# Optimization experiments

Hardware: AMD Instinct MI355X
Metric: run time of the kernel (lower is better)

The kernel has to match this reference:

```python
import jax, jax.numpy as jnp
import numpy as np

IN_FEATURES = 4096
OUT_FEATURES = 4096
INQ = IN_FEATURES // 4
OUTQ = OUT_FEATURES // 4


def setup_inputs() -> dict:
    key = jax.random.key(0)
    kx, krr, kri, krj, krk, kb = jax.random.split(key, 6)
    scale = 1.0 / np.sqrt(INQ)
    x = jax.random.normal(kx, (8192, IN_FEATURES), dtype=jnp.float32)
    W_rr = jax.random.uniform(krr, (OUTQ, INQ), jnp.float32, -scale, scale)
    # ri/rj/rk weights are scaled by 0.5 at init in the original module
    W_ri = jax.random.uniform(kri, (OUTQ, INQ), jnp.float32, -scale, scale) * 0.5
    W_rj = jax.random.uniform(krj, (OUTQ, INQ), jnp.float32, -scale, scale) * 0.5
    W_rk = jax.random.uniform(krk, (OUTQ, INQ), jnp.float32, -scale, scale) * 0.5
    b_rr = jax.random.uniform(kb, (OUTQ,), jnp.float32, -scale, scale)
    return {"x": x, "W_rr": W_rr, "W_ri": W_ri, "W_rj": W_rj, "W_rk": W_rk, "b_rr": b_rr}


def reference(x, W_rr, W_ri, W_rj, W_rk, b_rr):
    B, F = x.shape
    q = F // 4
    # Stack the four quaternion components: Xc[c] = component c, shape (4, B, q)
    Xc = x.reshape(B, 4, q).transpose(1, 0, 2)
    # Apply each quarter-sized linear to all four components at once.
    Rr = jnp.einsum('cbi,oi->cbo', Xc, W_rr) + b_rr  # linear_rr (with bias)
    Ri = jnp.einsum('cbi,oi->cbo', Xc, W_ri)         # linear_ri
    Rj = jnp.einsum('cbi,oi->cbo', Xc, W_rj)         # linear_rj
    Rk = jnp.einsum('cbi,oi->cbo', Xc, W_rk)         # linear_rk
    # Hamilton-product style combination
    out_r = Rr[0] - Ri[1] - Rj[2] - Rk[3]
    out_i = Ri[0] + Rr[1] + Rk[2] - Rj[3]
    out_j = Rj[0] - Rk[1] + Rr[2] + Ri[3]
    out_k = Rk[0] + Rj[1] - Ri[2] + Rr[3]
    # torch.stack(dim=1).view(B,-1) == concat along features
    return jnp.concatenate([out_r, out_i, out_j, out_k], axis=1)
```

## Files before the change

kernel.cpp:

```cpp
#include <hip/hip_runtime.h>
#include <hip/hip_bf16.h>
#include <stdint.h>

#define M_DIM 8192
#define K_DIM 4096
#define N_DIM 4096
#define QO 1024
#define BM 256
#define BN 128
#define BK 32
#define FBM 128
#define FBN 128

typedef __bf16 bf16x8_t __attribute__((ext_vector_type(8)));
typedef float f32x4_t __attribute__((ext_vector_type(4)));

__device__ __forceinline__ uint32_t f2bf_rne(float f) {
    union { float f; uint32_t u; } v; v.f = f;
    return (v.u + 0x7FFFu + ((v.u >> 16) & 1u)) >> 16;
}
__device__ __forceinline__ uint32_t pack2bf(float lo, float hi) {
    return f2bf_rne(lo) | (f2bf_rne(hi) << 16);
}

__global__ __launch_bounds__(256) void cvt_x_kernel(const float* __restrict__ x,
                                                    uint16_t* __restrict__ xb, int n8) {
    int i = blockIdx.x * 256 + threadIdx.x;
    if (i >= n8) return;
    float4 v0 = ((const float4*)x)[2 * i];
    float4 v1 = ((const float4*)x)[2 * i + 1];
    uint4 o;
    o.x = pack2bf(v0.x, v0.y);
    o.y = pack2bf(v0.z, v0.w);
    o.z = pack2bf(v1.x, v1.y);
    o.w = pack2bf(v1.z, v1.w);
    ((uint4*)xb)[i] = o;
}

__global__ __launch_bounds__(256) void build_w_kernel(
    const float* __restrict__ wrr, const float* __restrict__ wri,
    const float* __restrict__ wrj, const float* __restrict__ wrk,
    uint16_t* __restrict__ wb, int n8) {
    int g = blockIdx.x * 256 + threadIdx.x;
    if (g >= n8) return;
    int n  = g >> 9;
    int k8 = (g & 511) << 3;
    int cp = n >> 10, o = n & 1023;
    int c  = k8 >> 10, i = k8 & 1023;
    int tsel = cp ^ c;
    const float* w = (tsel == 0) ? wrr : (tsel == 1) ? wri : (tsel == 2) ? wrj : wrk;
    float s = ((0x428Eu >> ((cp << 2) | c)) & 1u) ? -1.0f : 1.0f;
    const float* p = w + (size_t)o * QO + i;
    float4 v0 = ((const float4*)p)[0];
    float4 v1 = ((const float4*)p)[1];
    uint4 ob;
    ob.x = pack2bf(s * v0.x, s * v0.y);
    ob.y = pack2bf(s * v0.z, s * v0.w);
    ob.z = pack2bf(s * v1.x, s * v1.y);
    ob.w = pack2bf(s * v1.z, s * v1.w);
    ((uint4*)wb)[g] = ob;
}

__global__ __launch_bounds__(256, 2) void qgemm256_kernel(
    const uint16_t* __restrict__ Abf, const uint16_t* __restrict__ Bbf,
    const float* __restrict__ bias, float* __restrict__ C)
{
    __shared__ uint16_t lA[BM * BK];
    __shared__ uint16_t lB[BN * BK];
    const int t    = threadIdx.x;
    const int wave = t >> 6;
    const int lane = t & 63;
    const int bn = blockIdx.x, bm = blockIdx.y;
    const int wm = wave >> 1, wn = wave & 1;

    f32x4_t acc[8][4];
#pragma unroll
    for (int a = 0; a < 8; ++a)
#pragma unroll
        for (int b = 0; b < 4; ++b)
            acc[a][b] = (f32x4_t){0.f, 0.f, 0.f, 0.f};

    const int fr  = lane & 15;
    const int fkb = (lane >> 4) << 3;
    const uint16_t* pA[8];
    const uint16_t* pB[4];
#pragma unroll
    for (int i = 0; i < 8; ++i)
        pA[i] = lA + (wm * 128 + i * 16 + fr) * BK + fkb;
#pragma unroll
    for (int i = 0; i < 4; ++i)
        pB[i] = lB + (wn * 64 + i * 16 + fr) * BK + fkb;

    const int srow = lane >> 2;
    const int scol = (lane & 3) << 3;
    const uint16_t* gA0 = Abf + (size_t)(bm * BM + wave * 64 + srow) * K_DIM + scol;
    const uint16_t* gB0 = Bbf + (size_t)(bn * BN + wave * 32 + srow) * K_DIM + scol;
    uint16_t* lA0 = lA + wave * 64 * BK;
    uint16_t* lB0 = lB + wave * 32 * BK;

#pragma unroll 1
    for (int kb = 0; kb < K_DIM; kb += BK) {
#pragma unroll
        for (int i = 0; i < 4; ++i)
            __builtin_amdgcn_global_load_lds(
                (const __attribute__((address_space(1))) void*)(gA0 + (size_t)i * 16 * K_DIM + kb),
                (__attribute__((address_space(3))) void*)(lA0 + i * 16 * BK), 16, 0, 0);
#pragma unroll
        for (int i = 0; i < 2; ++i)
            __builtin_amdgcn_global_load_lds(
                (const __attribute__((address_space(1))) void*)(gB0 + (size_t)i * 16 * K_DIM + kb),
                (__attribute__((address_space(3))) void*)(lB0 + i * 16 * BK), 16, 0, 0);
        __syncthreads();

        bf16x8_t bfr[4];
#pragma unroll
        for (int i = 0; i < 4; ++i)
            bfr[i] = *(const bf16x8_t*)pB[i];
#pragma unroll
        for (int mi = 0; mi < 8; ++mi) {
            bf16x8_t af = *(const bf16x8_t*)pA[mi];
#pragma unroll
            for (int ni = 0; ni < 4; ++ni)
                acc[mi][ni] = __builtin_amdgcn_mfma_f32_16x16x32_bf16(
                    af, bfr[ni], acc[mi][ni], 0, 0, 0);
        }
        __syncthreads();
    }

    const int row0 = bm * BM + wm * 128 + ((lane >> 4) << 2);
    const int col0 = bn * BN + wn * 64 + (lane & 15);
#pragma unroll
    for (int ni = 0; ni < 4; ++ni) {
        const int col = col0 + ni * 16;
        const float bv = bias[col & (QO - 1)];
#pragma unroll
        for (int mi = 0; mi < 8; ++mi) {
            const int r = row0 + mi * 16;
            float* cptr = C + (size_t)r * N_DIM + col;
#pragma unroll
            for (int rr = 0; rr < 4; ++rr)
                cptr[(size_t)rr * N_DIM] = acc[mi][ni][rr] + bv;
        }
    }
}

__global__ __launch_bounds__(256) void qgemm_fb_kernel(
    const float* __restrict__ x,
    const float* __restrict__ wrr, const float* __restrict__ wri,
    const float* __restrict__ wrj, const float* __restrict__ wrk,
    const float* __restrict__ bias, float* __restrict__ C)
{
    __shared__ uint16_t lA[FBM * BK];
    __shared__ uint16_t lB[FBN * BK];
    const int t    = threadIdx.x;
    const int wave = t >> 6;
    const int lane = t & 63;
    const int bn = blockIdx.x, bm = blockIdx.y;
    const int wm = wave >> 1, wn = wave & 1;

    f32x4_t acc[4][4];
#pragma unroll
    for (int a = 0; a < 4; ++a)
#pragma unroll
        for (int b = 0; b < 4; ++b)
            acc[a][b] = (f32x4_t){0.f, 0.f, 0.f, 0.f};

    const int fr  = lane & 15;
    const int fkb = (lane >> 4) << 3;
    const uint16_t* pA[4];
    const uint16_t* pB[4];
#pragma unroll
    for (int i = 0; i < 4; ++i) {
        pA[i] = lA + (wm * 64 + i * 16 + fr) * BK + fkb;
        pB[i] = lB + (wn * 64 + i * 16 + fr) * BK + fkb;
    }

    const int mr = t >> 1;
    const int mc = (t & 1) << 4;
    int ng = bn * FBN + mr;
    int bcp = ng >> 10;
    int bo  = ng & 1023;

#pragma unroll 1
    for (int kb = 0; kb < K_DIM; kb += BK) {
        const float* pa = x + (size_t)(bm * FBM + mr) * K_DIM + kb + mc;
        float4 a0 = ((const float4*)pa)[0], a1 = ((const float4*)pa)[1],
               a2 = ((const float4*)pa)[2], a3 = ((const float4*)pa)[3];
        uint4 wv0 = make_uint4(pack2bf(a0.x, a0.y), pack2bf(a0.z, a0.w),
                               pack2bf(a1.x, a1.y), pack2bf(a1.z, a1.w));
        uint4 wv1 = make_uint4(pack2bf(a2.x, a2.y), pack2bf(a2.z, a2.w),
                               pack2bf(a3.x, a3.y), pack2bf(a3.z, a3.w));
        *(uint4*)(lA + mr * BK + mc)     = wv0;
        *(uint4*)(lA + mr * BK + mc + 8) = wv1;

        int k0 = kb + mc;
        int c  = k0 >> 10, ii = k0 & 1023;
        int tsel = bcp ^ c;
        const float* w = (tsel == 0) ? wrr : (tsel == 1) ? wri : (tsel == 2) ? wrj : wrk;
        float s = ((0x428Eu >> ((bcp << 2) | c)) & 1u) ? -1.0f : 1.0f;
        const float* pb = w + (size_t)bo * QO + ii;
        float4 b0 = ((const float4*)pb)[0], b1 = ((const float4*)pb)[1],
               b2 = ((const float4*)pb)[2], b3 = ((const float4*)pb)[3];
        uint4 u0 = make_uint4(pack2bf(s * b0.x, s * b0.y), pack2bf(s * b0.z, s * b0.w),
                              pack2bf(s * b1.x, s * b1.y), pack2bf(s * b1.z, s * b1.w));
        uint4 u1 = make_uint4(pack2bf(s * b2.x, s * b2.y), pack2bf(s * b2.z, s * b2.w),
                              pack2bf(s * b3.x, s * b3.y), pack2bf(s * b3.z, s * b3.w));
        *(uint4*)(lB + mr * BK + mc)     = u0;
        *(uint4*)(lB + mr * BK + mc + 8) = u1;
        __syncthreads();

        bf16x8_t af[4], bfr[4];
#pragma unroll
        for (int i = 0; i < 4; ++i) {
            af[i]  = *(const bf16x8_t*)pA[i];
            bfr[i] = *(const bf16x8_t*)pB[i];
        }
#pragma unroll
        for (int mi = 0; mi < 4; ++mi)
#pragma unroll
            for (int ni = 0; ni < 4; ++ni)
                acc[mi][ni] = __builtin_amdgcn_mfma_f32_16x16x32_bf16(
                    af[mi], bfr[ni], acc[mi][ni], 0, 0, 0);
        __syncthreads();
    }

    const int row0 = bm * FBM + wm * 64 + ((lane >> 4) << 2);
    const int col0 = bn * FBN + wn * 64 + (lane & 15);
#pragma unroll
    for (int ni = 0; ni < 4; ++ni) {
        const int col = col0 + ni * 16;
        const float bv = bias[col & (QO - 1)];
#pragma unroll
        for (int mi = 0; mi < 4; ++mi) {
            const int r = row0 + mi * 16;
            float* cptr = C + (size_t)r * N_DIM + col;
#pragma unroll
            for (int rr = 0; rr < 4; ++rr)
                cptr[(size_t)rr * N_DIM] = acc[mi][ni][rr] + bv;
        }
    }
}

extern "C" void kernel_launch(void* const* d_in, const int* in_sizes, int n_in,
                              void* d_out, int out_size, void* d_ws, size_t ws_size,
                              hipStream_t stream) {
    const float* x   = (const float*)d_in[0];
    const float* wrr = (const float*)d_in[1];
    const float* wri = (const float*)d_in[2];
    const float* wrj = (const float*)d_in[3];
    const float* wrk = (const float*)d_in[4];
    const float* brr = (const float*)d_in[5];
    float* out = (float*)d_out;

    const size_t xb_bytes = (size_t)M_DIM * K_DIM * 2;
    const size_t wb_bytes = (size_t)N_DIM * K_DIM * 2;

    if (ws_size >= xb_bytes + wb_bytes) {
        uint16_t* xb = (uint16_t*)d_ws;
        uint16_t* wb = (uint16_t*)((char*)d_ws + xb_bytes);
        const int nx8 = M_DIM * K_DIM / 8;
        cvt_x_kernel<<<nx8 / 256, 256, 0, stream>>>(x, xb, nx8);
        const int nw8 = N_DIM * K_DIM / 8;
        build_w_kernel<<<nw8 / 256, 256, 0, stream>>>(wrr, wri, wrj, wrk, wb, nw8);
        dim3 grid(N_DIM / BN, M_DIM / BM);
        qgemm256_kernel<<<grid, 256, 0, stream>>>(xb, wb, brr, out);
    } else {
        dim3 grid(N_DIM / FBN, M_DIM / FBM);
        qgemm_fb_kernel<<<grid, 256, 0, stream>>>(x, wrr, wri, wrj, wrk, brr, out);
    }
}
```

Measured before the change: 544.6 us.

## Rewrite bf16 GEMM as 256x256 double-buffered 8-wave pipelined kernel with swizzled LDS

Replaces the 256x128 single-buffered GEMM with a 512-thread 256x256x64 tile kernel. It double-buffers LDS with direct global-to-LDS loads split into four phases, interleaving fragment reads, next-tile staging and MFMA work, with s_setprio around the MFMAs. LDS addresses are XOR-swizzled to avoid bank conflicts, and a block-index swizzle improves L2 reuse. The two conversion kernels are merged into one launch. The cost is higher register and LDS pressure (128KB shared) and more complex barrier and waitcnt logic.

```diff
diff --git a/kernel.cpp b/kernel.cpp
--- a/kernel.cpp
+++ b/kernel.cpp
@@ -1,16 +1,22 @@
 #include <hip/hip_runtime.h>
-#include <hip/hip_bf16.h>
 #include <stdint.h>
 
 #define M_DIM 8192
 #define K_DIM 4096
 #define N_DIM 4096
 #define QO 1024
+
 #define BM 256
-#define BN 128
-#define BK 32
+#define BN 256
+#define BK 64
+#define NT (K_DIM / BK)
+#define GX (N_DIM / BN)
+#define GY (M_DIM / BM)
+#define NWG (GX * GY)
+
 #define FBM 128
 #define FBN 128
+#define FBK 32
 
 typedef __bf16 bf16x8_t __attribute__((ext_vector_type(8)));
 typedef float f32x4_t __attribute__((ext_vector_type(4)));
@@ -23,55 +29,132 @@
     return f2bf_rne(lo) | (f2bf_rne(hi) << 16);
 }
 
-__global__ __launch_bounds__(256) void cvt_x_kernel(const float* __restrict__ x,
-                                                    uint16_t* __restrict__ xb, int n8) {
-    int i = blockIdx.x * 256 + threadIdx.x;
-    if (i >= n8) return;
-    float4 v0 = ((const float4*)x)[2 * i];
-    float4 v1 = ((const float4*)x)[2 * i + 1];
-    uint4 o;
-    o.x = pack2bf(v0.x, v0.y);
-    o.y = pack2bf(v0.z, v0.w);
-    o.z = pack2bf(v1.x, v1.y);
-    o.w = pack2bf(v1.z, v1.w);
-    ((uint4*)xb)[i] = o;
-}
-
-__global__ __launch_bounds__(256) void build_w_kernel(
+#define NXB (M_DIM * K_DIM / 8 / 256)
+#define NWB (N_DIM * K_DIM / 8 / 256)
+
+__global__ __launch_bounds__(256) void prep_kernel(
+    const float* __restrict__ x,
     const float* __restrict__ wrr, const float* __restrict__ wri,
     const float* __restrict__ wrj, const float* __restrict__ wrk,
-    uint16_t* __restrict__ wb, int n8) {
-    int g = blockIdx.x * 256 + threadIdx.x;
-    if (g >= n8) return;
-    int n  = g >> 9;
-    int k8 = (g & 511) << 3;
-    int cp = n >> 10, o = n & 1023;
-    int c  = k8 >> 10, i = k8 & 1023;
-    int tsel = cp ^ c;
-    const float* w = (tsel == 0) ? wrr : (tsel == 1) ? wri : (tsel == 2) ? wrj : wrk;
-    float s = ((0x428Eu >> ((cp << 2) | c)) & 1u) ? -1.0f : 1.0f;
-    const float* p = w + (size_t)o * QO + i;
-    float4 v0 = ((const float4*)p)[0];
-    float4 v1 = ((const float4*)p)[1];
-    uint4 ob;
-    ob.x = pack2bf(s * v0.x, s * v0.y);
-    ob.y = pack2bf(s * v0.z, s * v0.w);
-    ob.z = pack2bf(s * v1.x, s * v1.y);
-    ob.w = pack2bf(s * v1.z, s * v1.w);
-    ((uint4*)wb)[g] = ob;
-}
-
-__global__ __launch_bounds__(256, 2) void qgemm256_kernel(
+    uint16_t* __restrict__ xb, uint16_t* __restrict__ wb)
+{
+    const int bid = blockIdx.x;
+    if (bid < NXB) {
+        const int i = bid * 256 + threadIdx.x;
+        float4 v0 = ((const float4*)x)[2 * i];
+        float4 v1 = ((const float4*)x)[2 * i + 1];
+        uint4 o;
+        o.x = pack2bf(v0.x, v0.y);
+        o.y = pack2bf(v0.z, v0.w);
+        o.z = pack2bf(v1.x, v1.y);
+        o.w = pack2bf(v1.z, v1.w);
+        ((uint4*)xb)[i] = o;
+    } else {
+        const int g = (bid - NXB) * 256 + threadIdx.x;
+        const int n  = g >> 9;
+        const int k8 = (g & 511) << 3;
+        const int cp = n >> 10, o = n & 1023;
+        const int c  = k8 >> 10, i = k8 & 1023;
+        const int tsel = cp ^ c;
+        const float* w = (tsel == 0) ? wrr : (tsel == 1) ? wri : (tsel == 2) ? wrj : wrk;
+        const float s = ((0x428Eu >> ((cp << 2) | c)) & 1u) ? -1.0f : 1.0f;
+        const float* p = w + (size_t)o * QO + i;
+        float4 v0 = ((const float4*)p)[0];
+        float4 v1 = ((const float4*)p)[1];
+        uint4 ob;
+        ob.x = pack2bf(s * v0.x, s * v0.y);
+        ob.y = pack2bf(s * v0.z, s * v0.w);
+        ob.z = pack2bf(s * v1.x, s * v1.y);
+        ob.w = pack2bf(s * v1.z, s * v1.w);
+        ((uint4*)wb)[g] = ob;
+    }
+}
+
+
+#define STAGE(bufEl, abEl, h, kb, G, RB) do {                                   \
+    uint16_t* _d = sm + (bufEl) + (abEl) + (h) * 8192 + wid * 1024;             \
+    const uint16_t* _g0 = (G) + (size_t)((RB) + (h) * 128 + sr0) * K_DIM + (kb) + sc0; \
+    const uint16_t* _g1 = (G) + (size_t)((RB) + (h) * 128 + sr1) * K_DIM + (kb) + sc1; \
+    __builtin_amdgcn_global_load_lds(                                           \
+        (const __attribute__((address_space(1))) void*)_g0,                     \
+        (__attribute__((address_space(3))) void*)_d, 16, 0, 0);                 \
+    __builtin_amdgcn_global_load_lds(                                           \
+        (const __attribute__((address_space(1))) void*)_g1,                     \
+        (__attribute__((address_space(3))) void*)(_d + 512), 16, 0, 0);         \
+} while (0)
+
+#define LDA(mh) do {                                                            \
+    const char* _b = sR + aBase + (mh) * 8192;                                  \
+    _Pragma("unroll") for (int _m = 0; _m < 4; ++_m) {                          \
+        af[_m][0] = *(const bf16x8_t*)(_b + _m * 2048 + ko0);                   \
+        af[_m][1] = *(const bf16x8_t*)(_b + _m * 2048 + ko1);                   \
+    }                                                                           \
+} while (0)
+
+#define LDB(nh) do {                                                            \
+    const char* _b = sR + bBase;                                                \
+    _Pragma("unroll") for (int _n = 0; _n < 2; ++_n) {                          \
+        bfr[(nh) * 2 + _n][0] = *(const bf16x8_t*)(_b + ((nh) * 2 + _n) * 2048 + ko0); \
+        bfr[(nh) * 2 + _n][1] = *(const bf16x8_t*)(_b + ((nh) * 2 + _n) * 2048 + ko1); \
+    }                                                                           \
+} while (0)
+
+#define MM(mh, nh) do {                                                         \
+    _Pragma("unroll") for (int _ks = 0; _ks < 2; ++_ks)                         \
+    _Pragma("unroll") for (int _m = 0; _m < 4; ++_m)                            \
+    _Pragma("unroll") for (int _n = 0; _n < 2; ++_n)                            \
+        acc[(mh) * 4 + _m][(nh) * 2 + _n] =                                     \
+            __builtin_amdgcn_mfma_f32_16x16x32_bf16(                            \
+                af[_m][_ks], bfr[(nh) * 2 + _n][_ks],                           \
+                acc[(mh) * 4 + _m][(nh) * 2 + _n], 0, 0, 0);                    \
+} while (0)
+
+#define FENCE() asm volatile("" ::: "memory")
+
+#define PH(READS, STAGES, MFMAS, VM) do {                                       \
+    READS;                                                                      \
+    STAGES;                                                                     \
+    FENCE();                                                                    \
+    __builtin_amdgcn_s_barrier();                                               \
+    asm volatile("s_waitcnt lgkmcnt(0)" ::: "memory");                          \
+    __builtin_amdgcn_s_setprio(1);                                              \
+    MFMAS;                                                                      \
+    __builtin_amdgcn_s_setprio(0);                                              \
+    VM;                                                                         \
+    FENCE();                                                                    \
+    __builtin_amdgcn_s_barrier();                                               \
+    FENCE();                                                                    \
+} while (0)
+
+__global__ __launch_bounds__(512, 2) void qgemm8p_kernel(
     const uint16_t* __restrict__ Abf, const uint16_t* __restrict__ Bbf,
     const float* __restrict__ bias, float* __restrict__ C)
 {
-    __shared__ uint16_t lA[BM * BK];
-    __shared__ uint16_t lB[BN * BK];
-    const int t    = threadIdx.x;
-    const int wave = t >> 6;
-    const int lane = t & 63;
-    const int bn = blockIdx.x, bm = blockIdx.y;
-    const int wm = wave >> 1, wn = wave & 1;
+    __shared__ __align__(16) uint16_t sm[65536];
+
+    const int tid  = threadIdx.x;
+    const int wid  = tid >> 6;
+    const int lane = tid & 63;
+    const int wm = wid >> 2, wn = wid & 3;
+
+    const int flat = blockIdx.x;
+    const int swb  = ((flat & 7) << 6) | (flat >> 3);
+    const int bm = swb >> 4, bn = swb & 15;
+    const int aRow = bm * BM, bRow = bn * BN;
+
+    const int o0   = wid * 2048 + lane * 16;
+    const int swzS = ((lane >> 3) & 7) << 4;
+    const int lin0 = o0 ^ swzS;
+    const int sr0 = lin0 >> 7, sc0 = (lin0 & 127) >> 1;
+    const int sr1 = sr0 + 8,   sc1 = sc0;
+
+    const int fr  = lane & 15;
+    const int q16 = ((lane >> 4) & 3) << 4;
+    const int ko0 = q16 ^ ((fr & 7) << 4);
+    const int ko1 = ko0 ^ 64;
+    const int aBase = wm * 16384 + fr * 128;
+    const int bBase = 32768 + (wn >> 1) * 16384 + (wn & 1) * 8192 + fr * 128;
+    const char* const smc = (const char*)sm;
 
     f32x4_t acc[8][4];
 #pragma unroll
@@ -80,51 +163,50 @@
         for (int b = 0; b < 4; ++b)
             acc[a][b] = (f32x4_t){0.f, 0.f, 0.f, 0.f};
 
-    const int fr  = lane & 15;
-    const int fkb = (lane >> 4) << 3;
-    const uint16_t* pA[8];
-    const uint16_t* pB[4];
-#pragma unroll
-    for (int i = 0; i < 8; ++i)
-        pA[i] = lA + (wm * 128 + i * 16 + fr) * BK + fkb;
-#pragma unroll
-    for (int i = 0; i < 4; ++i)
-        pB[i] = lB + (wn * 64 + i * 16 + fr) * BK + fkb;
-
-    const int srow = lane >> 2;
-    const int scol = (lane & 3) << 3;
-    const uint16_t* gA0 = Abf + (size_t)(bm * BM + wave * 64 + srow) * K_DIM + scol;
-    const uint16_t* gB0 = Bbf + (size_t)(bn * BN + wave * 32 + srow) * K_DIM + scol;
-    uint16_t* lA0 = lA + wave * 64 * BK;
-    uint16_t* lB0 = lB + wave * 32 * BK;
-
+    bf16x8_t af[4][2];
+    bf16x8_t bfr[4][2];
+
+    STAGE(0,     16384, 0, 0,  Bbf, bRow);
+    STAGE(0,     16384, 1, 0,  Bbf, bRow);
+    STAGE(0,     0,     0, 0,  Abf, aRow);
+    STAGE(0,     0,     1, 0,  Abf, aRow);
+    STAGE(32768, 16384, 0, BK, Bbf, bRow);
+    STAGE(32768, 16384, 1, BK, Bbf, bRow);
+    asm volatile("s_waitcnt vmcnt(4)" ::: "memory");
+    __builtin_amdgcn_s_barrier();
+    FENCE();
+
+    int bufR = 0;
 #pragma unroll 1
-    for (int kb = 0; kb < K_DIM; kb += BK) {
-#pragma unroll
-        for (int i = 0; i < 4; ++i)
-            __builtin_amdgcn_global_load_lds(
-                (const __attribute__((address_space(1))) void*)(gA0 + (size_t)i * 16 * K_DIM + kb),
-                (__attribute__((address_space(3))) void*)(lA0 + i * 16 * BK), 16, 0, 0);
-#pragma unroll
-        for (int i = 0; i < 2; ++i)
-            __builtin_amdgcn_global_load_lds(
-                (const __attribute__((address_space(1))) void*)(gB0 + (size_t)i * 16 * K_DIM + kb),
-                (__attribute__((address_space(3))) void*)(lB0 + i * 16 * BK), 16, 0, 0);
-        __syncthreads();
-
-        bf16x8_t bfr[4];
-#pragma unroll
-        for (int i = 0; i < 4; ++i)
-            bfr[i] = *(const bf16x8_t*)pB[i];
-#pragma unroll
-        for (int mi = 0; mi < 8; ++mi) {
-            bf16x8_t af = *(const bf16x8_t*)pA[mi];
-#pragma unroll
-            for (int ni = 0; ni < 4; ++ni)
-                acc[mi][ni] = __builtin_amdgcn_mfma_f32_16x16x32_bf16(
-                    af, bfr[ni], acc[mi][ni], 0, 0, 0);
-        }
-        __syncthreads();
+    for (int t = 0; t < NT - 2; ++t) {
+        const int bufW = 32768 - bufR;
+        const char* sR = smc + bufR * 2;
+        const int kb1 = (t + 1) * BK;
+        const int kb2 = (t + 2) * BK;
+        PH(LDA(0); LDB(0), STAGE(bufW, 0, 0, kb1, Abf, aRow), MM(0, 0), (void)0);
+        PH(LDB(1),         STAGE(bufW, 0, 1, kb1, Abf, aRow), MM(0, 1), (void)0);
+        PH(LDA(1),         STAGE(bufR, 16384, 0, kb2, Bbf, bRow), MM(1, 1), (void)0);
+        PH((void)0,        STAGE(bufR, 16384, 1, kb2, Bbf, bRow), MM(1, 0),
+           asm volatile("s_waitcnt vmcnt(4)" ::: "memory"));
+        bufR = bufW;
+    }
+    {
+        const int bufW = 32768 - bufR;
+        const char* sR = smc + bufR * 2;
+        const int kb1 = (NT - 1) * BK;
+        PH(LDA(0); LDB(0), STAGE(bufW, 0, 0, kb1, Abf, aRow), MM(0, 0), (void)0);
+        PH(LDB(1),         STAGE(bufW, 0, 1, kb1, Abf, aRow), MM(0, 1), (void)0);
+        PH(LDA(1),         (void)0,                           MM(1, 1), (void)0);
+        PH((void)0,        (void)0,                           MM(1, 0),
+           asm volatile("s_waitcnt vmcnt(0)" ::: "memory"));
+        bufR = bufW;
+    }
+    {
+        const char* sR = smc + bufR * 2;
+        PH(LDA(0); LDB(0), (void)0, MM(0, 0), (void)0);
+        PH(LDB(1),         (void)0, MM(0, 1), (void)0);
+        PH(LDA(1),         (void)0, MM(1, 1), (void)0);
+        PH((void)0,        (void)0, MM(1, 0), (void)0);
     }
 
     const int row0 = bm * BM + wm * 128 + ((lane >> 4) << 2);
@@ -135,8 +217,7 @@
         const float bv = bias[col & (QO - 1)];
 #pragma unroll
         for (int mi = 0; mi < 8; ++mi) {
-            const int r = row0 + mi * 16;
-            float* cptr = C + (size_t)r * N_DIM + col;
+            float* cptr = C + (size_t)(row0 + mi * 16) * N_DIM + col;
 #pragma unroll
             for (int rr = 0; rr < 4; ++rr)
                 cptr[(size_t)rr * N_DIM] = acc[mi][ni][rr] + bv;
@@ -150,8 +231,8 @@
     const float* __restrict__ wrj, const float* __restrict__ wrk,
     const float* __restrict__ bias, float* __restrict__ C)
 {
-    __shared__ uint16_t lA[FBM * BK];
-    __shared__ uint16_t lB[FBN * BK];
+    __shared__ uint16_t lA[FBM * FBK];
+    __shared__ uint16_t lB[FBN * FBK];
     const int t    = threadIdx.x;
     const int wave = t >> 6;
     const int lane = t & 63;
@@ -171,8 +252,8 @@
     const uint16_t* pB[4];
 #pragma unroll
     for (int i = 0; i < 4; ++i) {
-        pA[i] = lA + (wm * 64 + i * 16 + fr) * BK + fkb;
-        pB[i] = lB + (wn * 64 + i * 16 + fr) * BK + fkb;
+        pA[i] = lA + (wm * 64 + i * 16 + fr) * FBK + fkb;
+        pB[i] = lB + (wn * 64 + i * 16 + fr) * FBK + fkb;
     }
 
     const int mr = t >> 1;
@@ -182,7 +263,7 @@
     int bo  = ng & 1023;
 
 #pragma unroll 1
-    for (int kb = 0; kb < K_DIM; kb += BK) {
+    for (int kb = 0; kb < K_DIM; kb += FBK) {
         const float* pa = x + (size_t)(bm * FBM + mr) * K_DIM + kb + mc;
         float4 a0 = ((const float4*)pa)[0], a1 = ((const float4*)pa)[1],
                a2 = ((const float4*)pa)[2], a3 = ((const float4*)pa)[3];
@@ -190,8 +271,8 @@
                                pack2bf(a1.x, a1.y), pack2bf(a1.z, a1.w));
         uint4 wv1 = make_uint4(pack2bf(a2.x, a2.y), pack2bf(a2.z, a2.w),
                                pack2bf(a3.x, a3.y), pack2bf(a3.z, a3.w));
-        *(uint4*)(lA + mr * BK + mc)     = wv0;
-        *(uint4*)(lA + mr * BK + mc + 8) = wv1;
+        *(uint4*)(lA + mr * FBK + mc)     = wv0;
+        *(uint4*)(lA + mr * FBK + mc + 8) = wv1;
 
         int k0 = kb + mc;
         int c  = k0 >> 10, ii = k0 & 1023;
@@ -205,22 +286,22 @@
                               pack2bf(s * b1.x, s * b1.y), pack2bf(s * b1.z, s * b1.w));
         uint4 u1 = make_uint4(pack2bf(s * b2.x, s * b2.y), pack2bf(s * b2.z, s * b2.w),
                               pack2bf(s * b3.x, s * b3.y), pack2bf(s * b3.z, s * b3.w));
-        *(uint4*)(lB + mr * BK + mc)     = u0;
-        *(uint4*)(lB + mr * BK + mc + 8) = u1;
+        *(uint4*)(lB + mr * FBK + mc)     = u0;
+        *(uint4*)(lB + mr * FBK + mc + 8) = u1;
         __syncthreads();
 
-        bf16x8_t af[4], bfr[4];
+        bf16x8_t afr[4], bfrg[4];
 #pragma unroll
         for (int i = 0; i < 4; ++i) {
-            af[i]  = *(const bf16x8_t*)pA[i];
-            bfr[i] = *(const bf16x8_t*)pB[i];
+            afr[i]  = *(const bf16x8_t*)pA[i];
+            bfrg[i] = *(const bf16x8_t*)pB[i];
         }
 #pragma unroll
         for (int mi = 0; mi < 4; ++mi)
 #pragma unroll
             for (int ni = 0; ni < 4; ++ni)
                 acc[mi][ni] = __builtin_amdgcn_mfma_f32_16x16x32_bf16(
-                    af[mi], bfr[ni], acc[mi][ni], 0, 0, 0);
+                    afr[mi], bfrg[ni], acc[mi][ni], 0, 0, 0);
         __syncthreads();
     }
 
@@ -258,12 +339,8 @@
     if (ws_size >= xb_bytes + wb_bytes) {
         uint16_t* xb = (uint16_t*)d_ws;
         uint16_t* wb = (uint16_t*)((char*)d_ws + xb_bytes);
-        const int nx8 = M_DIM * K_DIM / 8;
-        cvt_x_kernel<<<nx8 / 256, 256, 0, stream>>>(x, xb, nx8);
-        const int nw8 = N_DIM * K_DIM / 8;
-        build_w_kernel<<<nw8 / 256, 256, 0, stream>>>(wrr, wri, wrj, wrk, wb, nw8);
-        dim3 grid(N_DIM / BN, M_DIM / BM);
-        qgemm256_kernel<<<grid, 256, 0, stream>>>(xb, wb, brr, out);
+        prep_kernel<<<NXB + NWB, 256, 0, stream>>>(x, wrr, wri, wrj, wrk, xb, wb);
+        qgemm8p_kernel<<<dim3(NWG), dim3(512), 0, stream>>>(xb, wb, brr, out);
     } else {
         dim3 grid(N_DIM / FBN, M_DIM / FBM);
         qgemm_fb_kernel<<<grid, 256, 0, stream>>>(x, wrr, wri, wrj, wrk, brr, out);
```

Measured after the change: 461.0 us. -15.4%, faster.
